# Kernel optimization log

Measured on AMD Instinct MI355X. Metric: run time of the kernel, lower is better.

Reference implementation:

```python
import jax, jax.numpy as jnp
import numpy as np

N_NODES = 50000
N_EDGES = 300000
HID = 256


def setup_inputs() -> dict:
    key = jax.random.key(0)
    ks = jax.random.split(key, 8)
    s = lambda fan_in: 1.0 / np.sqrt(fan_in)
    return {
        "node_embeddings": jax.random.normal(ks[0], (N_NODES, HID), dtype=jnp.float32),
        "edge_index": jax.random.randint(ks[1], (2, N_EDGES), 0, N_NODES, dtype=jnp.int64),
        "edge_attr": jax.random.normal(ks[2], (N_EDGES, 3), dtype=jnp.float32),
        "W1": jax.random.normal(ks[3], (2 * HID + 3, HID), dtype=jnp.float32) * s(2 * HID + 3),
        "b1": jnp.zeros((HID,), dtype=jnp.float32),
        "W2": jax.random.normal(ks[4], (HID, HID // 2), dtype=jnp.float32) * s(HID),
        "b2": jnp.zeros((HID // 2,), dtype=jnp.float32),
        "W3": jax.random.normal(ks[5], (HID // 2, HID // 4), dtype=jnp.float32) * s(HID // 2),
        "b3": jnp.zeros((HID // 4,), dtype=jnp.float32),
        "W4": jax.random.normal(ks[6], (HID // 4, 3), dtype=jnp.float32) * s(HID // 4),
        "b4": jnp.zeros((3,), dtype=jnp.float32),
    }


def reference(node_embeddings, edge_index, edge_attr, W1, b1, W2, b2, W3, b3, W4, b4):
    # Gather source/target node embeddings: [E, H] each
    src = node_embeddings[edge_index[0]]
    dst = node_embeddings[edge_index[1]]
    feats = jnp.concatenate([src, dst, edge_attr], axis=-1)  # [E, 2H+3]
    # edge_encoder: Linear -> ReLU -> (Dropout=identity in eval) -> Linear
    h = jax.nn.relu(feats @ W1 + b1)
    h = h @ W2 + b2  # [E, H//2]
    # classifier: Linear -> ReLU -> Linear
    h = jax.nn.relu(h @ W3 + b3)
    logits = h @ W4 + b4  # [E, 3]
    return logits
```

## Files before the change

kernel.cpp:

```cpp
#include <hip/hip_runtime.h>
#include <hip/hip_bf16.h>
#include <stdint.h>
#include <stddef.h>


#define NN 50000
#define NE 300000
#define KG(kq,g2) ((kq)*2+(g2))
#define NBG1 782

using bf16x8 = __attribute__((ext_vector_type(8))) short;
using f32x16 = __attribute__((ext_vector_type(16))) float;
using f32x4  = __attribute__((ext_vector_type(4))) float;
using f32x2  = __attribute__((ext_vector_type(2))) float;
using u32x4  = __attribute__((ext_vector_type(4))) unsigned int;
using u32x2  = __attribute__((ext_vector_type(2))) unsigned int;

#define OFF_PQ   0ULL
#define SZ_PQ    (50000ULL*512ULL*2ULL)
#define OFF_W1   (OFF_PQ + SZ_PQ)
#define SZ_W1    (512ULL*256ULL*2ULL)
#define OFF_W1C  (OFF_W1 + SZ_W1)
#define SZ_W1C   (3ULL*256ULL*4ULL)
#define OFF_W2   (OFF_W1C + SZ_W1C)
#define SZ_W2    (128ULL*256ULL*2ULL)
#define OFF_W3   (OFF_W2 + SZ_W2)
#define SZ_W3    (64ULL*128ULL*2ULL)
#define OFF_W4   (OFF_W3 + SZ_W3)
#define SZ_W4    (16ULL*64ULL*2ULL)
#define OFF_FLAG (OFF_W4 + SZ_W4)
#define WS_NEED  (OFF_FLAG + 16ULL)

__device__ __forceinline__ unsigned short f2bf(float x){
  unsigned u = __float_as_uint(x);
  unsigned r = 0x7FFFu + ((u >> 16) & 1u);
  return (unsigned short)((u + r) >> 16);
}
__device__ __forceinline__ unsigned cvtpk(float lo, float hi){
  unsigned r;
  asm("v_cvt_pk_bf16_f32 %0, %1, %2" : "=v"(r) : "v"(lo), "v"(hi));
  return r;
}
__device__ __forceinline__ f32x2 unpk(unsigned w){
  f32x2 r;
  r[0] = __uint_as_float(w << 16);
  r[1] = __uint_as_float(w & 0xFFFF0000u);
  return r;
}
__device__ __forceinline__ f32x16 mfma32(bf16x8 a, bf16x8 b, f32x16 c){
  return __builtin_amdgcn_mfma_f32_32x32x16_bf16(a, b, c, 0, 0, 0);
}
__device__ __forceinline__ f32x4 mfma16(bf16x8 a, bf16x8 b, f32x4 c){
  return __builtin_amdgcn_mfma_f32_16x16x32_bf16(a, b, c, 0, 0, 0);
}
__device__ __forceinline__ f32x16 zero16(){
  f32x16 v;
#pragma unroll
  for (int i = 0; i < 16; ++i) v[i] = 0.f;
  return v;
}

__global__ void prep_pack(const float* __restrict__ W1,
                          const int* __restrict__ ei32, char* __restrict__ ws)
{
  int i = blockIdx.x * 256 + threadIdx.x;
  unsigned short* w1i = (unsigned short*)(ws + OFF_W1);
  if (i < 131072){
    int out = i & 511;
    int kgj = i >> 9;
    int kg = kgj >> 3, j = kgj & 7;
    int k = (kg >> 1)*16 + (kg & 1)*8 + j;
    float v = (out < 256) ? W1[(size_t)k*256 + out]
                          : W1[(size_t)(256 + k)*256 + (out - 256)];
    w1i[((size_t)kg*512 + out)*8 + j] = f2bf(v);
  }
  if (i == 0){
    int f = 1;
    for (int t = 1; t < 64; t += 2) if (ei32[t] != 0) { f = 0; break; }
    *(int*)(ws + OFF_FLAG) = f;
  }
}

__global__ __launch_bounds__(512, 4) void gemm1(const float* __restrict__ emb,
                                                const float* __restrict__ b1,
                                                const float* __restrict__ W1,
                                                const float* __restrict__ W2,
                                                const float* __restrict__ W3,
                                                const float* __restrict__ W4,
                                                char* __restrict__ ws)
{
  __shared__ __align__(16) unsigned short U[16896];

  const int tid = threadIdx.x;
  const int bid = blockIdx.x;

  if (bid >= NBG1){
    int p = (bid - NBG1)*512 + tid;
    unsigned short* w2i = (unsigned short*)(ws + OFF_W2);
    unsigned short* w3i = (unsigned short*)(ws + OFF_W3);
    unsigned short* w4i = (unsigned short*)(ws + OFF_W4);
    float* w1c = (float*)(ws + OFF_W1C);
    if (p < 32768){
      int j = p & 7, out = (p >> 3) & 127, sg = p >> 10;
      int k = (sg >> 2)*32 + (sg & 3)*8 + j;
      w2i[p] = f2bf(W2[(size_t)k*128 + out]);
    } else if (p < 40960){
      int i3 = p - 32768;
      int j = i3 & 7, out = (i3 >> 3) & 63, sg = i3 >> 9;
      int k = (sg >> 2)*32 + (sg & 3)*8 + j;
      w3i[i3] = f2bf(W3[(size_t)k*64 + out]);
    } else if (p < 41984){
      int i4 = p - 40960;
      int j = i4 & 7, out = (i4 >> 3) & 15, sg = i4 >> 7;
      int k = (sg >> 2)*32 + (sg & 3)*8 + j;
      w4i[i4] = (out < 3) ? f2bf(W4[(size_t)k*3 + out]) : (unsigned short)0;
    } else if (p < 42752){
      int i5 = p - 41984;
      w1c[i5] = W1[(size_t)(512 + i5/256)*256 + (i5 & 255)];
    }
    return;
  }

  const int wv = tid >> 6, l = tid & 63, ln = l & 31, g2 = l >> 5;
  const int ob = wv * 64;
  const int nb = bid * 64;
  const unsigned short* w1L = (const unsigned short*)(ws + OFF_W1);
  unsigned short* PQ = (unsigned short*)(ws + OFF_PQ);

#pragma unroll
  for (int it = 0; it < 8; ++it){
    int u = it*512 + tid;
    int kg = u >> 7, node = (u >> 1) & 63, half = u & 1;
    int n = nb + node; if (n >= NN) n = NN - 1;
    int k = (kg >> 1)*16 + (kg & 1)*8 + half*4;
    f32x4 e = *(const f32x4*)(emb + (size_t)n*256 + k);
    u32x2 w; w[0] = cvtpk(e[0], e[1]); w[1] = cvtpk(e[2], e[3]);
    *(u32x2*)(U + (size_t)kg*512 + node*8 + half*4) = w;
  }

  bf16x8 awA0 = *(const bf16x8*)(w1L + ((size_t)KG(0,g2)*512 + ob +      ln)*8);
  bf16x8 awA1 = *(const bf16x8*)(w1L + ((size_t)KG(0,g2)*512 + ob + 32 + ln)*8);
  bf16x8 awB0 = *(const bf16x8*)(w1L + ((size_t)KG(1,g2)*512 + ob +      ln)*8);
  bf16x8 awB1 = *(const bf16x8*)(w1L + ((size_t)KG(1,g2)*512 + ob + 32 + ln)*8);

  __syncthreads();

  f32x16 acc[2][2];
  acc[0][0] = zero16(); acc[0][1] = zero16();
  acc[1][0] = zero16(); acc[1][1] = zero16();

#define G1STEP(KQ, W0, W1F)                                                    \
  {                                                                            \
    bf16x8 b0  = *(const bf16x8*)(U + ((size_t)KG(KQ,g2)*64 +      ln)*8);     \
    bf16x8 b1v = *(const bf16x8*)(U + ((size_t)KG(KQ,g2)*64 + 32 + ln)*8);     \
    bf16x8 a0 = W0, a1 = W1F;                                                  \
    if ((KQ) + 2 <= 15){                                                       \
      W0  = *(const bf16x8*)(w1L + ((size_t)KG((KQ)+2,g2)*512 + ob +      ln)*8); \
      W1F = *(const bf16x8*)(w1L + ((size_t)KG((KQ)+2,g2)*512 + ob + 32 + ln)*8); \
    }                                                                          \
    acc[0][0] = mfma32(a0, b0,  acc[0][0]);                                    \
    acc[1][0] = mfma32(a1, b0,  acc[1][0]);                                    \
    acc[0][1] = mfma32(a0, b1v, acc[0][1]);                                    \
    acc[1][1] = mfma32(a1, b1v, acc[1][1]);                                    \
  }
  G1STEP(0,  awA0, awA1);
  G1STEP(1,  awB0, awB1);
  G1STEP(2,  awA0, awA1);
  G1STEP(3,  awB0, awB1);
  G1STEP(4,  awA0, awA1);
  G1STEP(5,  awB0, awB1);
  G1STEP(6,  awA0, awA1);
  G1STEP(7,  awB0, awB1);
  G1STEP(8,  awA0, awA1);
  G1STEP(9,  awB0, awB1);
  G1STEP(10, awA0, awA1);
  G1STEP(11, awB0, awB1);
  G1STEP(12, awA0, awA1);
  G1STEP(13, awB0, awB1);
  G1STEP(14, awA0, awA1);
  G1STEP(15, awB0, awB1);
#undef G1STEP

  __syncthreads();

  const int r_ = tid >> 4;
  const int j_ = tid & 15;
#define G1PASS(BG)                                                             \
  {                                                                            \
    _Pragma("unroll")                                                          \
    for (int t2 = 0; t2 < 2; ++t2){                                            \
      _Pragma("unroll")                                                        \
      for (int rr = 0; rr < 4; ++rr){                                          \
        int o = ob + t2*32 + rr*8 + g2*4;                                      \
        f32x4 bv = {0.f,0.f,0.f,0.f};                                          \
        if (ob + t2*32 < 256) bv = *(const f32x4*)(b1 + o);                    \
        unsigned d0 = cvtpk(acc[t2][BG][rr*4+0]+bv[0], acc[t2][BG][rr*4+1]+bv[1]); \
        unsigned d1 = cvtpk(acc[t2][BG][rr*4+2]+bv[2], acc[t2][BG][rr*4+3]+bv[3]); \
        u32x2 st = {d0, d1};                                                   \
        *(u32x2*)(U + (size_t)ln*516 + o) = st;                                \
      }                                                                        \
    }                                                                          \
    __syncthreads();                                                           \
    {                                                                          \
      int n = nb + (BG)*32 + r_;                                               \
      if (n < NN){                                                             \
        _Pragma("unroll")                                                      \
        for (int ii = 0; ii < 4; ++ii){                                        \
          uint4 v = *(const uint4*)(U + (size_t)r_*516 + ii*128 + j_*8);       \
          *(uint4*)(PQ + (size_t)n*512 + ii*128 + j_*8) = v;                   \
        }                                                                      \
      }                                                                        \
    }                                                                          \
  }
  G1PASS(0);
  __syncthreads();
  G1PASS(1);
#undef G1PASS
}


#define PAIRX(LO, HI, D) ((D)==0 ? (f32x2){(LO)[0],(LO)[1]} : \
                          (D)==1 ? (f32x2){(LO)[2],(LO)[3]} : \
                          (D)==2 ? (f32x2){(HI)[0],(HI)[1]} : \
                                   (f32x2){(HI)[2],(HI)[3]})

#define H1BUILD(PC, QC, A0, A1, A2, BOUT)                                      \
  {                                                                            \
    u32x4 pu = __builtin_bit_cast(u32x4, PC);                                  \
    u32x4 qu = __builtin_bit_cast(u32x4, QC);                                  \
    f32x2 z2 = {0.f, 0.f};                                                     \
    unsigned bu0, bu1, bu2, bu3;                                               \
    _Pragma("unroll")                                                          \
    for (int d = 0; d < 4; ++d){                                               \
      f32x2 h = unpk(pu[d]) + unpk(qu[d]);                                     \
      h += PAIRX(w0lo, w0hi, d) * (A0);                                        \
      h += PAIRX(w1lo, w1hi, d) * (A1);                                        \
      h += PAIRX(w2lo, w2hi, d) * (A2);                                        \
      h = __builtin_elementwise_max(h, z2);                                    \
      unsigned c = cvtpk(h[0], h[1]);                                          \
      if (d==0) bu0 = c; else if (d==1) bu1 = c; else if (d==2) bu2 = c;       \
      else bu3 = c;                                                            \
    }                                                                          \
    u32x4 buv = {bu0, bu1, bu2, bu3};                                          \
    BOUT = __builtin_bit_cast(bf16x8, buv);                                    \
  }

#define L2S(S, P0, Q0, P1, Q1)                                                 \
  {                                                                            \
    const int kb = (S)*32 + g4*8;                                              \
    f32x4 w0lo = *(const f32x4*)(w1c_lds +   0 + kb);                          \
    f32x4 w0hi = *(const f32x4*)(w1c_lds +   4 + kb);                          \
    f32x4 w1lo = *(const f32x4*)(w1c_lds + 256 + kb);                          \
    f32x4 w1hi = *(const f32x4*)(w1c_lds + 260 + kb);                          \
    f32x4 w2lo = *(const f32x4*)(w1c_lds + 512 + kb);                          \
    f32x4 w2hi = *(const f32x4*)(w1c_lds + 516 + kb);                          \
    bf16x8 b0, b1;                                                             \
    H1BUILD(P0, Q0, at0e0, at1e0, at2e0, b0);                                  \
    H1BUILD(P1, Q1, at0e1, at1e1, at2e1, b1);                                  \
    if ((S) + 2 <= 7){                                                         \
      P0 = *(const bf16x8*)(Prow0 + ((S)+2)*32);                               \
      Q0 = *(const bf16x8*)(Qrow0 + ((S)+2)*32);                               \
      P1 = *(const bf16x8*)(Prow1 + ((S)+2)*32);                               \
      Q1 = *(const bf16x8*)(Qrow1 + ((S)+2)*32);                               \
    }                                                                          \
    const char* abase = smem + (size_t)((S)*4 + g4)*2048 + c16*16;             \
    _Pragma("unroll")                                                          \
    for (int t = 0; t < 8; ++t){                                               \
      bf16x8 af = *(const bf16x8*)(abase + t*256);                             \
      acc2[t][0] = mfma16(af, b0, acc2[t][0]);                                 \
      acc2[t][1] = mfma16(af, b1, acc2[t][1]);                                 \
    }                                                                          \
  }

__global__ __launch_bounds__(512, 4) void fused(const int* __restrict__ eidx,
                                                const float* __restrict__ attr,
                                                const float* __restrict__ b2,
                                                const float* __restrict__ b3,
                                                const float* __restrict__ b4,
                                                const char* __restrict__ ws,
                                                float* __restrict__ out)
{
  __shared__ __align__(16) char smem[65536 + 3072];
  const int tid = threadIdx.x;
  const int wv = tid >> 6, l = tid & 63, c16 = l & 15, g4 = l >> 4;

  const unsigned short* PQ  = (const unsigned short*)(ws + OFF_PQ);
  const unsigned short* w3g = (const unsigned short*)(ws + OFF_W3);
  const unsigned short* w4g = (const unsigned short*)(ws + OFF_W4);
  const float* W1c = (const float*)(ws + OFF_W1C);
  const int flag64 = *(const int*)(ws + OFF_FLAG);
  const float* w1c_lds = (const float*)(smem + 65536);

  const int ebase = blockIdx.x * 256 + wv * 32;
  const int e0 = ebase + c16,      e1 = ebase + 16 + c16;
  const bool ev0 = (e0 < NE),      ev1 = (e1 < NE);
  const int ec0 = ev0 ? e0 : 0,    ec1 = ev1 ? e1 : 0;
  const int si0 = flag64 ? eidx[2*(size_t)ec0]        : eidx[ec0];
  const int di0 = flag64 ? eidx[2*((size_t)NE + ec0)] : eidx[NE + ec0];
  const int si1 = flag64 ? eidx[2*(size_t)ec1]        : eidx[ec1];
  const int di1 = flag64 ? eidx[2*((size_t)NE + ec1)] : eidx[NE + ec1];

  const float at0e0 = ev0 ? attr[(size_t)ec0*3 + 0] : 0.f;
  const float at1e0 = ev0 ? attr[(size_t)ec0*3 + 1] : 0.f;
  const float at2e0 = ev0 ? attr[(size_t)ec0*3 + 2] : 0.f;
  const float at0e1 = ev1 ? attr[(size_t)ec1*3 + 0] : 0.f;
  const float at1e1 = ev1 ? attr[(size_t)ec1*3 + 1] : 0.f;
  const float at2e1 = ev1 ? attr[(size_t)ec1*3 + 2] : 0.f;

  const unsigned short* Prow0 = PQ + (size_t)si0*512 + g4*8;
  const unsigned short* Qrow0 = PQ + (size_t)di0*512 + 256 + g4*8;
  const unsigned short* Prow1 = PQ + (size_t)si1*512 + g4*8;
  const unsigned short* Qrow1 = PQ + (size_t)di1*512 + 256 + g4*8;

  bf16x8 pA0 = *(const bf16x8*)(Prow0 +  0), qA0 = *(const bf16x8*)(Qrow0 +  0);
  bf16x8 pA1 = *(const bf16x8*)(Prow1 +  0), qA1 = *(const bf16x8*)(Qrow1 +  0);
  bf16x8 pB0 = *(const bf16x8*)(Prow0 + 32), qB0 = *(const bf16x8*)(Qrow0 + 32);
  bf16x8 pB1 = *(const bf16x8*)(Prow1 + 32), qB1 = *(const bf16x8*)(Qrow1 + 32);

  {
    const uint4* src = (const uint4*)(ws + OFF_W2);
    uint4* dst = (uint4*)smem;
#pragma unroll
    for (int it = 0; it < 8; ++it) dst[it*512 + tid] = src[it*512 + tid];
    if (tid < 192) ((f32x4*)(smem + 65536))[tid] = ((const f32x4*)W1c)[tid];
  }
  __syncthreads();

  f32x4 acc2[8][2];
#pragma unroll
  for (int t = 0; t < 8; ++t){ acc2[t][0] = (f32x4){0,0,0,0}; acc2[t][1] = (f32x4){0,0,0,0}; }

  L2S(0, pA0, qA0, pA1, qA1);
  L2S(1, pB0, qB0, pB1, qB1);
  L2S(2, pA0, qA0, pA1, qA1);
  L2S(3, pB0, qB0, pB1, qB1);
  L2S(4, pA0, qA0, pA1, qA1);
  L2S(5, pB0, qB0, pB1, qB1);
  L2S(6, pA0, qA0, pA1, qA1);
  L2S(7, pB0, qB0, pB1, qB1);

  __syncthreads();

  unsigned short* hslot = (unsigned short*)(smem + wv*8192);
#pragma unroll
  for (int t = 0; t < 8; ++t){
    f32x4 bv = *(const f32x4*)(b2 + t*16 + g4*4);
    const int sg_o = t*2 + (g4 >> 1);
    const int j0 = (g4 & 1)*4;
#pragma unroll
    for (int g = 0; g < 2; ++g){
      unsigned d0 = cvtpk(acc2[t][g][0]+bv[0], acc2[t][g][1]+bv[1]);
      unsigned d1 = cvtpk(acc2[t][g][2]+bv[2], acc2[t][g][3]+bv[3]);
      u32x2 st = {d0, d1};
      *(u32x2*)(hslot + ((sg_o*32 + g*16 + c16)*8 + j0)) = st;
    }
  }

  f32x4 acc3[4][2];
#pragma unroll
  for (int t = 0; t < 4; ++t){ acc3[t][0] = (f32x4){0,0,0,0}; acc3[t][1] = (f32x4){0,0,0,0}; }
#pragma unroll
  for (int ks = 0; ks < 4; ++ks){
    const int sg = ks*4 + g4;
    bf16x8 bb0 = *(const bf16x8*)(hslot + (sg*32 +      c16)*8);
    bf16x8 bb1 = *(const bf16x8*)(hslot + (sg*32 + 16 + c16)*8);
#pragma unroll
    for (int t = 0; t < 4; ++t){
      bf16x8 af = *(const bf16x8*)(w3g + ((size_t)sg*64 + t*16 + c16)*8);
      acc3[t][0] = mfma16(af, bb0, acc3[t][0]);
      acc3[t][1] = mfma16(af, bb1, acc3[t][1]);
    }
  }

#pragma unroll
  for (int t = 0; t < 4; ++t){
    f32x4 bv = *(const f32x4*)(b3 + t*16 + g4*4);
    const int sg_o = t*2 + (g4 >> 1);
    const int j0 = (g4 & 1)*4;
#pragma unroll
    for (int g = 0; g < 2; ++g){
      unsigned d0 = cvtpk(fmaxf(acc3[t][g][0]+bv[0],0.f), fmaxf(acc3[t][g][1]+bv[1],0.f));
      unsigned d1 = cvtpk(fmaxf(acc3[t][g][2]+bv[2],0.f), fmaxf(acc3[t][g][3]+bv[3],0.f));
      u32x2 st = {d0, d1};
      *(u32x2*)(hslot + ((sg_o*32 + g*16 + c16)*8 + j0)) = st;
    }
  }

  f32x4 acc40 = {0,0,0,0}, acc41 = {0,0,0,0};
#pragma unroll
  for (int ks = 0; ks < 2; ++ks){
    const int sg = ks*4 + g4;
    bf16x8 af = *(const bf16x8*)(w4g + ((size_t)sg*16 + c16)*8);
    bf16x8 bb0 = *(const bf16x8*)(hslot + (sg*32 +      c16)*8);
    bf16x8 bb1 = *(const bf16x8*)(hslot + (sg*32 + 16 + c16)*8);
    acc40 = mfma16(af, bb0, acc40);
    acc41 = mfma16(af, bb1, acc41);
  }
  if (g4 == 0){
    float c0 = b4[0], c1 = b4[1], c2 = b4[2];
    if (ev0){
      out[(size_t)e0*3 + 0] = acc40[0] + c0;
      out[(size_t)e0*3 + 1] = acc40[1] + c1;
      out[(size_t)e0*3 + 2] = acc40[2] + c2;
    }
    if (ev1){
      out[(size_t)e1*3 + 0] = acc41[0] + c0;
      out[(size_t)e1*3 + 1] = acc41[1] + c1;
      out[(size_t)e1*3 + 2] = acc41[2] + c2;
    }
  }
}

extern "C" void kernel_launch(void* const* d_in, const int* in_sizes, int n_in,
                              void* d_out, int out_size, void* d_ws, size_t ws_size,
                              hipStream_t stream)
{
  const float* emb  = (const float*)d_in[0];
  const int*   eidx = (const int*)  d_in[1];
  const float* attr = (const float*)d_in[2];
  const float* W1   = (const float*)d_in[3];
  const float* b1   = (const float*)d_in[4];
  const float* W2   = (const float*)d_in[5];
  const float* b2   = (const float*)d_in[6];
  const float* W3   = (const float*)d_in[7];
  const float* b3   = (const float*)d_in[8];
  const float* W4   = (const float*)d_in[9];
  const float* b4   = (const float*)d_in[10];
  char* ws = (char*)d_ws;
  float* out = (float*)d_out;

  if (ws_size < WS_NEED) return;

  prep_pack<<<512, 256, 0, stream>>>(W1, eidx, ws);
  gemm1<<<NBG1 + 84, 512, 0, stream>>>(emb, b1, W1, W2, W3, W4, ws);
  fused<<<(NE + 255)/256, 512, 0, stream>>>(eidx, attr, b2, b3, b4, ws, out);
}
```

Before: 107.1 us.

## Bucket-sort edges by source node to improve gather locality in fused kernel

Adds histogram, scan and scatter kernels that build a permutation of edges grouped by source-node bucket (128 nodes per bucket). The fused kernel then processes edges in that order and writes outputs to the original edge positions. The aim is better cache reuse of the gathered P rows for source nodes. The cost is three extra launches, atomics, an extra indirection, and scattered output writes. The new path runs only if the workspace is large enough.

Measured after the change: 325.9 us. 204% more time.

```diff
diff --git a/kernel.cpp b/kernel.cpp
--- a/kernel.cpp
+++ b/kernel.cpp
@@ -8,6 +8,7 @@
 #define NE 300000
 #define KG(kq,g2) ((kq)*2+(g2))
 #define NBG1 782
+#define NBKT 391
 
 using bf16x8 = __attribute__((ext_vector_type(8))) short;
 using f32x16 = __attribute__((ext_vector_type(16))) float;
@@ -30,6 +31,10 @@
 #define SZ_W4    (16ULL*64ULL*2ULL)
 #define OFF_FLAG (OFF_W4 + SZ_W4)
 #define WS_NEED  (OFF_FLAG + 16ULL)
+#define OFF_HIST (WS_NEED)
+#define OFF_CURS (OFF_HIST + 2048ULL)
+#define OFF_PERM (OFF_CURS + 2048ULL)
+#define WS_NEED2 (OFF_PERM + (size_t)NE*4ULL)
 
 __device__ __forceinline__ unsigned short f2bf(float x){
   unsigned u = __float_as_uint(x);
@@ -74,11 +79,46 @@
                           : W1[(size_t)(256 + k)*256 + (out - 256)];
     w1i[((size_t)kg*512 + out)*8 + j] = f2bf(v);
   }
+  if (i < 512) ((int*)(ws + OFF_HIST))[i] = 0;
   if (i == 0){
     int f = 1;
     for (int t = 1; t < 64; t += 2) if (ei32[t] != 0) { f = 0; break; }
     *(int*)(ws + OFF_FLAG) = f;
   }
+}
+
+__global__ void ehist(const int* __restrict__ eidx, char* __restrict__ ws)
+{
+  int e = blockIdx.x*256 + threadIdx.x;
+  if (e >= NE) return;
+  const int flag64 = *(const int*)(ws + OFF_FLAG);
+  int si = flag64 ? eidx[2*(size_t)e] : eidx[e];
+  atomicAdd((int*)(ws + OFF_HIST) + (si >> 7), 1);
+}
+__global__ void escan(char* __restrict__ ws)
+{
+  __shared__ int s[512];
+  int t = threadIdx.x;
+  int* hist = (int*)(ws + OFF_HIST);
+  int v = (t < NBKT) ? hist[t] : 0;
+  s[t] = v;
+  __syncthreads();
+  for (int off = 1; off < 512; off <<= 1){
+    int add = (t >= off) ? s[t - off] : 0;
+    __syncthreads();
+    s[t] += add;
+    __syncthreads();
+  }
+  if (t < NBKT) ((int*)(ws + OFF_CURS))[t] = s[t] - v;
+}
+__global__ void escatter(const int* __restrict__ eidx, char* __restrict__ ws)
+{
+  int e = blockIdx.x*256 + threadIdx.x;
+  if (e >= NE) return;
+  const int flag64 = *(const int*)(ws + OFF_FLAG);
+  int si = flag64 ? eidx[2*(size_t)e] : eidx[e];
+  int pos = atomicAdd((int*)(ws + OFF_CURS) + (si >> 7), 1);
+  ((int*)(ws + OFF_PERM))[pos] = e;
 }
 
 __global__ __launch_bounds__(512, 4) void gemm1(const float* __restrict__ emb,
@@ -278,7 +318,8 @@
                                                 const float* __restrict__ b3,
                                                 const float* __restrict__ b4,
                                                 const char* __restrict__ ws,
-                                                float* __restrict__ out)
+                                                float* __restrict__ out,
+                                                const int use_perm)
 {
   __shared__ __align__(16) char smem[65536 + 3072];
   const int tid = threadIdx.x;
@@ -292,9 +333,17 @@
   const float* w1c_lds = (const float*)(smem + 65536);
 
   const int ebase = blockIdx.x * 256 + wv * 32;
-  const int e0 = ebase + c16,      e1 = ebase + 16 + c16;
-  const bool ev0 = (e0 < NE),      ev1 = (e1 < NE);
-  const int ec0 = ev0 ? e0 : 0,    ec1 = ev1 ? e1 : 0;
+  const int r0 = ebase + c16,      r1 = ebase + 16 + c16;
+  const bool ev0 = (r0 < NE),      ev1 = (r1 < NE);
+  int ec0, ec1;
+  if (use_perm){
+    const int* perm = (const int*)(ws + OFF_PERM);
+    ec0 = perm[ev0 ? r0 : 0];
+    ec1 = perm[ev1 ? r1 : 0];
+  } else {
+    ec0 = ev0 ? r0 : 0;
+    ec1 = ev1 ? r1 : 0;
+  }
   const int si0 = flag64 ? eidx[2*(size_t)ec0]        : eidx[ec0];
   const int di0 = flag64 ? eidx[2*((size_t)NE + ec0)] : eidx[NE + ec0];
   const int si1 = flag64 ? eidx[2*(size_t)ec1]        : eidx[ec1];
@@ -399,14 +448,14 @@
   if (g4 == 0){
     float c0 = b4[0], c1 = b4[1], c2 = b4[2];
     if (ev0){
-      out[(size_t)e0*3 + 0] = acc40[0] + c0;
-      out[(size_t)e0*3 + 1] = acc40[1] + c1;
-      out[(size_t)e0*3 + 2] = acc40[2] + c2;
+      out[(size_t)ec0*3 + 0] = acc40[0] + c0;
+      out[(size_t)ec0*3 + 1] = acc40[1] + c1;
+      out[(size_t)ec0*3 + 2] = acc40[2] + c2;
     }
     if (ev1){
-      out[(size_t)e1*3 + 0] = acc41[0] + c0;
-      out[(size_t)e1*3 + 1] = acc41[1] + c1;
-      out[(size_t)e1*3 + 2] = acc41[2] + c2;
+      out[(size_t)ec1*3 + 0] = acc41[0] + c0;
+      out[(size_t)ec1*3 + 1] = acc41[1] + c1;
+      out[(size_t)ec1*3 + 2] = acc41[2] + c2;
     }
   }
 }
@@ -430,8 +479,14 @@
   float* out = (float*)d_out;
 
   if (ws_size < WS_NEED) return;
+  const int use_perm = (ws_size >= WS_NEED2) ? 1 : 0;
 
   prep_pack<<<512, 256, 0, stream>>>(W1, eidx, ws);
+  if (use_perm){
+    ehist<<<(NE + 255)/256, 256, 0, stream>>>(eidx, ws);
+    escan<<<1, 512, 0, stream>>>(ws);
+    escatter<<<(NE + 255)/256, 256, 0, stream>>>(eidx, ws);
+  }
   gemm1<<<NBG1 + 84, 512, 0, stream>>>(emb, b1, W1, W2, W3, W4, ws);
-  fused<<<(NE + 255)/256, 512, 0, stream>>>(eidx, attr, b2, b3, b4, ws, out);
-}
+  fused<<<(NE + 255)/256, 512, 0, stream>>>(eidx, attr, b2, b3, b4, ws, out, use_perm);
+}
```
